# Optimization experiments

Measured on AMD Instinct MI355X. Metric: run time of the kernel, lower is better.

## Reference

```python
import jax, jax.numpy as jnp
import numpy as np

N_OBJECTS = 32  # mask labels 1..32 (0 = background)


def setup_inputs() -> dict:
    key = jax.random.key(0)
    k1, k2, k3, k4 = jax.random.split(key, 4)
    B, F, H, W = 8, 64, 256, 256
    encoded = jax.random.normal(k1, (B, F, H, W), dtype=jnp.float32)
    masks = jax.random.randint(k2, (B, 1, H, W), 0, N_OBJECTS + 1, dtype=jnp.int32)
    W1 = jax.random.normal(k3, (2 * F, F // 2), dtype=jnp.float32) * 0.05
    b1 = jnp.zeros((F // 2,), dtype=jnp.float32)
    W2 = jax.random.normal(k4, (F // 2, 4), dtype=jnp.float32) * 0.05
    b2 = jnp.zeros((4,), dtype=jnp.float32)
    return {"encoded": encoded, "masks": masks, "W1": W1, "b1": b1, "W2": W2, "b2": b2}


def reference(encoded, masks, W1, b1, W2, b2):
    B, F, H, W = encoded.shape
    # --- masked per-object max-pool (segment max over pixels) ---
    enc = encoded.reshape(B, F, H * W).transpose(0, 2, 1)  # [B, HW, F]
    ids = masks.reshape(B, H * W)                          # [B, HW]
    seg_max = jax.vmap(
        lambda d, i: jax.ops.segment_max(d, i, num_segments=N_OBJECTS + 1)
    )(enc, ids)                                            # [B, N+1, F]
    vectors = seg_max[:, 1:, :]                            # [B, N, F] (skip label 0)

    # --- O(N^2) pairwise MLP: connections[b,c,j,i] = sigmoid(MLP([v_i; v_j])) ---
    N = vectors.shape[1]
    vi = jnp.broadcast_to(vectors[:, :, None, :], (B, N, N, F))  # v_i over axis 1
    vj = jnp.broadcast_to(vectors[:, None, :, :], (B, N, N, F))  # v_j over axis 2
    pairs = jnp.concatenate([vi, vj], axis=-1)                   # [B, N, N, 2F]
    h = jnp.einsum('bijd,dh->bijh', pairs, W1) + b1
    out = jax.nn.sigmoid(jnp.einsum('bijh,hc->bijc', h, W2) + b2)  # [B, Ni, Nj, C]
    connections = out.transpose(0, 3, 2, 1)                        # [B, C, Nj, Ni]
    return vectors, connections
```

## Files before the change

kernel.cpp:

```cpp
#include <hip/hip_runtime.h>
#include <math.h>

#define B_      8
#define F_      64
#define HW_     65536
#define NSEG    33
#define NOBJ    32
#define FPB     4
#define FGRP    (F_ / FPB)
#define SLICES  32
#define PIXB    (HW_ / SLICES)
#define ENC_NEG_INF 0x007FFFFFu

__device__ __forceinline__ unsigned enc_f(float x) {
    unsigned u = __float_as_uint(x);
    return u ^ ((unsigned)((int)u >> 31) | 0x80000000u);
}
__device__ __forceinline__ float dec_f(unsigned e) {
    unsigned x = (e & 0x80000000u) ? (e ^ 0x80000000u) : ~e;
    return __uint_as_float(x);
}


__global__ __launch_bounds__(256, 8) void segmax_kernel(
        const float* __restrict__ enc, const int* __restrict__ masks,
        float* __restrict__ part) {
    __shared__ unsigned acc[FPB * NSEG * 32];
    const int tid = threadIdx.x;
    const int blk = blockIdx.x;
    const int b     = blk >> 9;
    const int fg    = (blk >> 5) & 15;
    const int slice = blk & 31;

    for (int i = tid; i < FPB * NSEG * 32; i += 256) acc[i] = ENC_NEG_INF;
    __syncthreads();

    const int fl   = tid >> 6;
    const int lane = tid & 63;
    unsigned* a = acc + fl * (NSEG * 32) + (lane & 31);

    const float4* ep = (const float4*)(enc + ((size_t)(b * F_ + fg * FPB + fl)) * HW_
                                       + slice * PIXB) + lane;
    const int4*   mp = (const int4*)(masks + (size_t)b * HW_ + slice * PIXB) + lane;

    #pragma unroll 4
    for (int c = 0; c < PIXB / 256; ++c) {
        float4 v  = ep[c * 64];
        int4   id = mp[c * 64];
        atomicMax(a + id.x * 32, enc_f(v.x));
        atomicMax(a + id.y * 32, enc_f(v.y));
        atomicMax(a + id.z * 32, enc_f(v.z));
        atomicMax(a + id.w * 32, enc_f(v.w));
    }
    __syncthreads();

    float* dst = part + (((size_t)b * SLICES + slice) * NSEG) * F_;
    for (int cell = tid; cell < FPB * NSEG; cell += 256) {
        int f = cell & 3, s = cell >> 2;
        const unsigned* row = acc + f * (NSEG * 32) + s * 32;
        unsigned m = ENC_NEG_INF;
        #pragma unroll
        for (int k = 0; k < 32; k += 4) {
            uint4 q = *(const uint4*)(row + k);
            unsigned m1 = q.x > q.y ? q.x : q.y;
            unsigned m2 = q.z > q.w ? q.z : q.w;
            unsigned m3 = m1 > m2 ? m1 : m2;
            m = m > m3 ? m : m3;
        }
        dst[s * F_ + fg * FPB + f] = dec_f(m);
    }
}

__global__ __launch_bounds__(256) void mlp_kernel(
        const float* __restrict__ part,
        const float* __restrict__ W1, const float* __restrict__ b1,
        const float* __restrict__ W2, const float* __restrict__ b2,
        float* __restrict__ out_vec, float* __restrict__ out_conn) {
    const int b   = blockIdx.x >> 2;
    const int it  = blockIdx.x & 3;
    const int tid = threadIdx.x;
    __shared__ float v[NOBJ * 65];
    __shared__ float w1s[2 * F_ * 32];
    __shared__ float w2s[32 * 4];
    __shared__ float b1s[32];
    __shared__ float Am[8 * 36];
    __shared__ float Bm[NOBJ * 36];

    for (int i = tid; i < 2 * F_ * 32 / 4; i += 256)
        ((float4*)w1s)[i] = ((const float4*)W1)[i];
    if (tid < 32) { w2s[tid*4+0]=W2[tid*4+0]; w2s[tid*4+1]=W2[tid*4+1];
                    w2s[tid*4+2]=W2[tid*4+2]; w2s[tid*4+3]=W2[tid*4+3];
                    b1s[tid] = b1[tid]; }

    for (int cell = tid; cell < NOBJ * F_; cell += 256) {
        int s = (cell >> 6) + 1, f = cell & 63;
        float m = -INFINITY;
        #pragma unroll 8
        for (int sl = 0; sl < SLICES; ++sl)
            m = fmaxf(m, part[(((size_t)b * SLICES + sl) * NSEG + s) * F_ + f]);
        v[(s - 1) * 65 + f] = m;
        if (it == 0) out_vec[b * NOBJ * F_ + cell] = m;
    }
    __syncthreads();

    for (int d = tid; d < 320; d += 256) {
        int kg, obj, half;
        if (d < 64) { half = 0; obj = it * 8 + (d >> 3); kg = d & 7; }
        else        { half = 1; obj = (d - 64) >> 3;     kg = d & 7; }
        const float* vv = v + obj * 65;
        const float* w  = w1s + half * (F_ * 32) + kg * 4;
        float4 s4 = {0.f, 0.f, 0.f, 0.f};
        #pragma unroll
        for (int f = 0; f < F_; ++f) {
            float4 wf = *(const float4*)(w + f * 32);
            float x = vv[f];
            s4.x = fmaf(x, wf.x, s4.x); s4.y = fmaf(x, wf.y, s4.y);
            s4.z = fmaf(x, wf.z, s4.z); s4.w = fmaf(x, wf.w, s4.w);
        }
        if (half == 0) {
            float4 bb = *(const float4*)(b1s + kg * 4);
            s4.x += bb.x; s4.y += bb.y; s4.z += bb.z; s4.w += bb.w;
            *(float4*)(Am + (d >> 3) * 36 + kg * 4) = s4;
        } else {
            *(float4*)(Bm + obj * 36 + kg * 4) = s4;
        }
    }
    __syncthreads();

    {
        int i_loc = tid >> 5, j = tid & 31;
        float o0 = b2[0], o1 = b2[1], o2 = b2[2], o3 = b2[3];
        #pragma unroll
        for (int kg = 0; kg < 8; ++kg) {
            float4 ha = *(const float4*)(Am + i_loc * 36 + kg * 4);
            float4 hb = *(const float4*)(Bm + j * 36 + kg * 4);
            float h0 = ha.x + hb.x, h1 = ha.y + hb.y;
            float h2 = ha.z + hb.z, h3 = ha.w + hb.w;
            const float* w2 = w2s + kg * 16;
            o0 = fmaf(h0, w2[0],  fmaf(h1, w2[4],  fmaf(h2, w2[8],  fmaf(h3, w2[12], o0))));
            o1 = fmaf(h0, w2[1],  fmaf(h1, w2[5],  fmaf(h2, w2[9],  fmaf(h3, w2[13], o1))));
            o2 = fmaf(h0, w2[2],  fmaf(h1, w2[6],  fmaf(h2, w2[10], fmaf(h3, w2[14], o2))));
            o3 = fmaf(h0, w2[3],  fmaf(h1, w2[7],  fmaf(h2, w2[11], fmaf(h3, w2[15], o3))));
        }
        float* oc = out_conn + (size_t)b * 4 * NOBJ * NOBJ + j * NOBJ + (it * 8 + i_loc);
        oc[0 * NOBJ * NOBJ] = 1.f / (1.f + expf(-o0));
        oc[1 * NOBJ * NOBJ] = 1.f / (1.f + expf(-o1));
        oc[2 * NOBJ * NOBJ] = 1.f / (1.f + expf(-o2));
        oc[3 * NOBJ * NOBJ] = 1.f / (1.f + expf(-o3));
    }
}

extern "C" void kernel_launch(void* const* d_in, const int* in_sizes, int n_in,
                              void* d_out, int out_size, void* d_ws, size_t ws_size,
                              hipStream_t stream) {
    const float* enc   = (const float*)d_in[0];
    const int*   masks = (const int*)  d_in[1];
    const float* W1    = (const float*)d_in[2];
    const float* b1    = (const float*)d_in[3];
    const float* W2    = (const float*)d_in[4];
    const float* b2    = (const float*)d_in[5];

    float* out_vec  = (float*)d_out;
    float* out_conn = out_vec + B_ * NOBJ * F_;
    float* part     = (float*)d_ws;

    segmax_kernel<<<B_ * FGRP * SLICES, 256, 0, stream>>>(enc, masks, part);
    mlp_kernel<<<B_ * 4, 256, 0, stream>>>(part, W1, b1, W2, b2, out_vec, out_conn);
}
```

Before: 255.6 us.

## Reuse mask loads across all features and reduce slices via global atomics

Each block now covers all 64 features for one pixel slice, so mask ids are loaded once into registers and reused across features instead of being reloaded per feature group. The 32-way replicated shared accumulators are dropped in favour of a single 64x33 table. Per-slice partial results are merged straight into the workspace with global atomicMax, guarded by a read, which a new init kernel fills beforehand. This removes the partial buffer and the 32-way slice reduction in the MLP kernel. The cost is more shared-memory atomic contention with no replication, an extra kernel launch, and fewer blocks (1024) each doing longer work.

```diff
diff --git a/kernel.cpp b/kernel.cpp
--- a/kernel.cpp
+++ b/kernel.cpp
@@ -6,10 +6,8 @@
 #define HW_     65536
 #define NSEG    33
 #define NOBJ    32
-#define FPB     4
-#define FGRP    (F_ / FPB)
-#define SLICES  32
-#define PIXB    (HW_ / SLICES)
+#define SLICES  128
+#define PXB     (HW_ / SLICES)
 #define ENC_NEG_INF 0x007FFFFFu
 
 __device__ __forceinline__ unsigned enc_f(float x) {
@@ -21,58 +19,57 @@
     return __uint_as_float(x);
 }
 
+__global__ void init_ws(unsigned* __restrict__ gws) {
+    int i = blockIdx.x * blockDim.x + threadIdx.x;
+    gws[i] = ENC_NEG_INF;
+}
 
-__global__ __launch_bounds__(256, 8) void segmax_kernel(
+__global__ __launch_bounds__(256, 4) void segmax_kernel(
         const float* __restrict__ enc, const int* __restrict__ masks,
-        float* __restrict__ part) {
-    __shared__ unsigned acc[FPB * NSEG * 32];
-    const int tid = threadIdx.x;
-    const int blk = blockIdx.x;
-    const int b     = blk >> 9;
-    const int fg    = (blk >> 5) & 15;
-    const int slice = blk & 31;
+        unsigned* __restrict__ gws) {
+    __shared__ unsigned acc[F_ * NSEG];
+    const int tid   = threadIdx.x;
+    const int b     = blockIdx.x >> 7;
+    const int slice = blockIdx.x & 127;
 
-    for (int i = tid; i < FPB * NSEG * 32; i += 256) acc[i] = ENC_NEG_INF;
+    for (int i = tid; i < F_ * NSEG; i += 256) acc[i] = ENC_NEG_INF;
+
+    const int wave = tid >> 6;
+    const int lane = tid & 63;
+
+    const int4* mp = (const int4*)(masks + (size_t)b * HW_ + slice * PXB);
+    int4 id0 = mp[lane];
+    int4 id1 = mp[lane + 64];
     __syncthreads();
 
-    const int fl   = tid >> 6;
-    const int lane = tid & 63;
-    unsigned* a = acc + fl * (NSEG * 32) + (lane & 31);
-
-    const float4* ep = (const float4*)(enc + ((size_t)(b * F_ + fg * FPB + fl)) * HW_
-                                       + slice * PIXB) + lane;
-    const int4*   mp = (const int4*)(masks + (size_t)b * HW_ + slice * PIXB) + lane;
-
+    const float* ebase = enc + ((size_t)(b * F_ + wave * 16)) * HW_ + slice * PXB;
     #pragma unroll 4
-    for (int c = 0; c < PIXB / 256; ++c) {
-        float4 v  = ep[c * 64];
-        int4   id = mp[c * 64];
-        atomicMax(a + id.x * 32, enc_f(v.x));
-        atomicMax(a + id.y * 32, enc_f(v.y));
-        atomicMax(a + id.z * 32, enc_f(v.z));
-        atomicMax(a + id.w * 32, enc_f(v.w));
+    for (int fo = 0; fo < 16; ++fo) {
+        const float4* ep = (const float4*)(ebase + (size_t)fo * HW_);
+        float4 v0 = ep[lane];
+        float4 v1 = ep[lane + 64];
+        unsigned* a = acc + (wave * 16 + fo) * NSEG;
+        atomicMax(a + id0.x, enc_f(v0.x));
+        atomicMax(a + id0.y, enc_f(v0.y));
+        atomicMax(a + id0.z, enc_f(v0.z));
+        atomicMax(a + id0.w, enc_f(v0.w));
+        atomicMax(a + id1.x, enc_f(v1.x));
+        atomicMax(a + id1.y, enc_f(v1.y));
+        atomicMax(a + id1.z, enc_f(v1.z));
+        atomicMax(a + id1.w, enc_f(v1.w));
     }
     __syncthreads();
 
-    float* dst = part + (((size_t)b * SLICES + slice) * NSEG) * F_;
-    for (int cell = tid; cell < FPB * NSEG; cell += 256) {
-        int f = cell & 3, s = cell >> 2;
-        const unsigned* row = acc + f * (NSEG * 32) + s * 32;
-        unsigned m = ENC_NEG_INF;
-        #pragma unroll
-        for (int k = 0; k < 32; k += 4) {
-            uint4 q = *(const uint4*)(row + k);
-            unsigned m1 = q.x > q.y ? q.x : q.y;
-            unsigned m2 = q.z > q.w ? q.z : q.w;
-            unsigned m3 = m1 > m2 ? m1 : m2;
-            m = m > m3 ? m : m3;
-        }
-        dst[s * F_ + fg * FPB + f] = dec_f(m);
+    unsigned* gb = gws + b * (NOBJ * F_);
+    for (int cell = tid; cell < NOBJ * F_; cell += 256) {
+        int s = (cell >> 6) + 1, f = cell & 63;
+        unsigned val = acc[f * NSEG + s];
+        if (val > gb[cell]) atomicMax(gb + cell, val);
     }
 }
 
 __global__ __launch_bounds__(256) void mlp_kernel(
-        const float* __restrict__ part,
+        const unsigned* __restrict__ gws,
         const float* __restrict__ W1, const float* __restrict__ b1,
         const float* __restrict__ W2, const float* __restrict__ b2,
         float* __restrict__ out_vec, float* __restrict__ out_conn) {
@@ -93,13 +90,9 @@
                     b1s[tid] = b1[tid]; }
 
     for (int cell = tid; cell < NOBJ * F_; cell += 256) {
-        int s = (cell >> 6) + 1, f = cell & 63;
-        float m = -INFINITY;
-        #pragma unroll 8
-        for (int sl = 0; sl < SLICES; ++sl)
-            m = fmaxf(m, part[(((size_t)b * SLICES + sl) * NSEG + s) * F_ + f]);
-        v[(s - 1) * 65 + f] = m;
-        if (it == 0) out_vec[b * NOBJ * F_ + cell] = m;
+        float m = dec_f(gws[b * (NOBJ * F_) + cell]);
+        v[(cell >> 6) * 65 + (cell & 63)] = m;
+        if (it == 0) out_vec[b * (NOBJ * F_) + cell] = m;
     }
     __syncthreads();
 
@@ -162,8 +155,9 @@
 
     float* out_vec  = (float*)d_out;
     float* out_conn = out_vec + B_ * NOBJ * F_;
-    float* part     = (float*)d_ws;
+    unsigned* gws   = (unsigned*)d_ws;
 
-    segmax_kernel<<<B_ * FGRP * SLICES, 256, 0, stream>>>(enc, masks, part);
-    mlp_kernel<<<B_ * 4, 256, 0, stream>>>(part, W1, b1, W2, b2, out_vec, out_conn);
+    init_ws<<<B_ * NOBJ * F_ / 256, 256, 0, stream>>>(gws);
+    segmax_kernel<<<B_ * SLICES, 256, 0, stream>>>(enc, masks, gws);
+    mlp_kernel<<<B_ * 4, 256, 0, stream>>>(gws, W1, b1, W2, b2, out_vec, out_conn);
 }
```

Result: faster. 231.9 us (-9.3%).
